# Optimization experiments

Measured on AMD Instinct MI355X. Metric: run time of the kernel, lower is better.

## Reference

```python
import jax, jax.numpy as jnp
import numpy as np

HEADS = 16
DIM_HEAD = 64
CHUNK = 64
EPS_LN = 1e-5
EPS_T5 = 1e-6


def _layernorm(x, g, b):
    mu = x.mean(-1, keepdims=True)
    var = x.var(-1, keepdims=True)
    return (x - mu) / jnp.sqrt(var + EPS_LN) * g + b


def _t5norm(x, w):
    # T5LayerNorm variant: divide by (||x|| * d^-0.5), i.e. RMS norm
    norm = jnp.linalg.norm(x, axis=-1, keepdims=True) * (x.shape[-1] ** -0.5)
    return x / jnp.maximum(norm, EPS_T5) * w


def _rotary(t, freqs):
    rot = freqs.shape[-1]
    t1, t2 = t[..., :rot], t[..., rot:]
    half = rot // 2
    a, b = t1[..., :half], t1[..., half:]
    rh = jnp.concatenate((-b, a), axis=-1)  # rotate_half
    t1 = t1 * jnp.cos(freqs) + rh * jnp.sin(freqs)
    return jnp.concatenate((t1, t2), axis=-1)


def _split_heads(t):
    B, N, _ = t.shape
    return t.reshape(B, N, HEADS, DIM_HEAD).transpose(0, 2, 1, 3)


def _merge_heads(t):
    B, H, N, D = t.shape
    return t.transpose(0, 2, 1, 3).reshape(B, N, H * D)


def _attend(q, k, v, causal=False):
    sim = jnp.einsum('bhid,bhjd->bhij', q, k)
    if causal:
        i, j = sim.shape[-2:]
        m = jnp.triu(jnp.ones((i, j), bool), j - i + 1)
        sim = jnp.where(m, jnp.finfo(sim.dtype).min, sim)
    attn = jax.nn.softmax(sim, axis=-1)
    return jnp.einsum('bhij,bhjd->bhid', attn, v)


def setup_inputs() -> dict:
    key = jax.random.key(0)
    ks = jax.random.split(key, 20)
    b, n, d = 4, 1024, 1024
    kc, r, rn = n // CHUNK, 2, 2 * CHUNK
    dff = 4 * d
    s = 0.02

    def W(i, *shape):
        return jax.random.normal(ks[i], shape, jnp.float32) * s

    return {
        'hidden_states': jax.random.normal(ks[0], (b, n, d), jnp.float32),
        'retrieval': jax.random.normal(ks[1], (b, kc, r, rn, d), jnp.float32),
        'q_pos_emb': jax.random.normal(ks[2], (1, 1, CHUNK, DIM_HEAD), jnp.float32),
        'k_pos_emb': jax.random.normal(ks[3], (1, 1, rn, DIM_HEAD), jnp.float32),
        'ln1_g': jnp.ones(d), 'ln1_b': jnp.zeros(d),
        'Wq_s': W(4, d, d), 'Wk_s': W(5, d, d), 'Wv_s': W(6, d, d),
        'Wo_s': W(7, d, d), 'bo_s': jnp.zeros(d),
        'ln2_g': jnp.ones(d), 'ln2_b': jnp.zeros(d),
        'Wq_c': W(8, d, d), 'Wk_c': W(9, d, d), 'Wv_c': W(10, d, d),
        'Wo_c': W(11, d, d), 'bo_c': jnp.zeros(d),
        'null_k': jax.random.normal(ks[12], (d,), jnp.float32),
        'null_v': jax.random.normal(ks[13], (d,), jnp.float32),
        'post_w': jnp.ones(d),
        'W1': W(14, d, dff), 'b1': jnp.zeros(dff),
        'W2': W(15, dff, d), 'b2': jnp.zeros(d),
    }


def reference(hidden_states, retrieval, q_pos_emb, k_pos_emb,
              ln1_g, ln1_b, Wq_s, Wk_s, Wv_s, Wo_s, bo_s,
              ln2_g, ln2_b, Wq_c, Wk_c, Wv_c, Wo_c, bo_c,
              null_k, null_v, post_w, W1, b1, W2, b2):
    b, n, d = hidden_states.shape
    scale = DIM_HEAD ** -0.5

    # --- causal self-attention (pre-LN) ---
    x = _layernorm(hidden_states, ln1_g, ln1_b)
    q = _split_heads(x @ Wq_s) * scale
    k = _split_heads(x @ Wk_s)
    v = _split_heads(x @ Wv_s)
    o = _merge_heads(_attend(q, k, v, causal=True)) @ Wo_s + bo_s
    hs = _layernorm(o + hidden_states, ln2_g, ln2_b)
    residual = hs  # residual taken after ln_2, before cross-attn (per source)

    # --- chunked cross-attention over retrieved neighbor chunks ---
    kc, r, rn = retrieval.shape[1:4]
    cp = CHUNK - 1  # causal padding
    seq_index = (n // CHUNK) * CHUNK
    # shift queries back by chunk_size-1 (causality), pad tail with zeros
    xq = jnp.pad(hs[:, cp:], ((0, 0), (0, cp), (0, 0)))[:, :seq_index]
    xq = xq.reshape(b * kc, CHUNK, d)
    ctx = retrieval.reshape(b * kc, r * rn, d)
    qpe = jnp.pad(q_pos_emb[:, :, cp:], ((0, 0), (0, 0), (0, cp), (0, 0)))
    kpe = jnp.tile(k_pos_emb, (1, 1, r, 1))  # 'b h n d -> b h (r n) d'
    q = _rotary(_split_heads(xq @ Wq_c) * scale, qpe)
    kk = _rotary(_split_heads(ctx @ Wk_c), kpe)
    vv = _split_heads(ctx @ Wv_c)
    nk = jnp.broadcast_to(null_k.reshape(1, HEADS, 1, DIM_HEAD), (b * kc, HEADS, 1, DIM_HEAD))
    nv = jnp.broadcast_to(null_v.reshape(1, HEADS, 1, DIM_HEAD), (b * kc, HEADS, 1, DIM_HEAD))
    kk = jnp.concatenate((nk, kk), axis=2)
    vv = jnp.concatenate((nv, vv), axis=2)
    cca = _merge_heads(_attend(q, kk, vv)) @ Wo_c + bo_c
    cca = cca.reshape(b, seq_index, d)
    # shift output forward by chunk_size-1, crop to n
    cca = jnp.pad(cca, ((0, 0), (cp, 0), (0, 0)))[:, :n]
    # PostNorm wrapper: T5 norm of (fn(x) + x)
    hs = _t5norm(cca + hs, post_w)

    # --- GPTNeo MLP (gelu-new / tanh approx) ---
    ff = jax.nn.gelu(hs @ W1 + b1, approximate=True) @ W2 + b2
    return residual + ff
```

## Files before the change

kernel.cpp:

```cpp
#include <hip/hip_runtime.h>
#include <hip/hip_bf16.h>
#include <math.h>

using u16 = unsigned short;

static constexpr int SEQ = 1024;
static constexpr int DM  = 1024;
static constexpr int DHD = 64;

typedef __bf16 bfv8 __attribute__((ext_vector_type(8)));
typedef float  f32x4 __attribute__((ext_vector_type(4)));

__device__ __forceinline__ float u2f(u16 u) {
  return __uint_as_float(((unsigned int)u) << 16);
}
__device__ __forceinline__ u16 f2b(float x) {
  __hip_bfloat16 h = __float2bfloat16(x);
  return *reinterpret_cast<u16*>(&h);
}
__device__ __forceinline__ void gload16(const u16* g, u16* l) {
  __builtin_amdgcn_global_load_lds(
      (const __attribute__((address_space(1))) unsigned int*)g,
      (__attribute__((address_space(3))) unsigned int*)l, 16, 0, 0);
}

template <int OT, bool HASBIAS, bool HASRES, bool DOGELU, bool ROT, int DBUF, int PART>
__global__ __launch_bounds__(256) void mgemm_k(
    const u16* __restrict__ A, const u16* __restrict__ Bt, void* __restrict__ C,
    int M, int K, int lda, int ldc, int coff, float alpha0, float alpha1, int acol,
    const float* __restrict__ bias, const float* __restrict__ res,
    const float* __restrict__ tab) {
  constexpr int NBUF = DBUF ? 2 : 1;
  __shared__ u16 As[NBUF][128 * 64];
  __shared__ u16 Bs[NBUF][128 * 64];
  const int tid = threadIdx.x;
  const int w = tid >> 6, lane = tid & 63;
  const int wr = w >> 1, wc = w & 1;
  const int koff = blockIdx.z * K;

  const int nwg = gridDim.x * gridDim.y;
  const int bid = blockIdx.y * gridDim.x + blockIdx.x;
  const int qq = nwg >> 3, r8 = nwg & 7;
  const int xcd = bid & 7, pos = bid >> 3;
  const int cbase = (xcd < r8) ? xcd * (qq + 1) : r8 * (qq + 1) + (xcd - r8) * qq;
  const int logical = cbase + pos;
  const int row0 = (logical / gridDim.x) << 7;
  const int col0 = (logical % gridDim.x) << 7;

  f32x4 acc[4][4] = {};

  auto STAGE = [&](int buf, int k0) {
#pragma unroll
    for (int i = 0; i < 4; ++i) {
      const int c = ((w << 2) + i) * 64 + lane;
      const int r = c >> 3;
      const int cbs = ((c & 7) ^ (r & 7)) << 3;
      const int r64 = r & 63;
      const int rB = (r & 64) | ((r64 & 15) << 2) | (r64 >> 4);
      gload16(A + (size_t)(row0 + r) * lda + koff + k0 + cbs, &As[buf][((w << 2) + i) << 9]);
      gload16(Bt + (size_t)(col0 + rB) * lda + koff + k0 + cbs, &Bs[buf][((w << 2) + i) << 9]);
    }
  };
  auto COMPUTE = [&](int buf) {
#pragma unroll
    for (int kk = 0; kk < 2; ++kk) {
      bfv8 af[4], bfr[4];
#pragma unroll
      for (int m = 0; m < 4; ++m) {
        const int ar = (wr << 6) + (m << 4) + (lane & 15);
        const int sl = ((kk << 2) | (lane >> 4)) ^ (ar & 7);
        af[m] = *reinterpret_cast<const bfv8*>(&As[buf][ar * 64 + (sl << 3)]);
      }
#pragma unroll
      for (int n = 0; n < 4; ++n) {
        const int br = (wc << 6) + (n << 4) + (lane & 15);
        const int sl = ((kk << 2) | (lane >> 4)) ^ (br & 7);
        bfr[n] = *reinterpret_cast<const bfv8*>(&Bs[buf][br * 64 + (sl << 3)]);
      }
#pragma unroll
      for (int m = 0; m < 4; ++m)
#pragma unroll
        for (int n = 0; n < 4; ++n)
          acc[m][n] = __builtin_amdgcn_mfma_f32_16x16x32_bf16(af[m], bfr[n], acc[m][n], 0, 0, 0);
    }
  };

  if constexpr (DBUF) {
    STAGE(0, 0);
    int cur = 0;
    for (int k0 = 0; k0 < K; k0 += 64) {
      if (k0 + 64 < K) {
        STAGE(cur ^ 1, k0 + 64);
        asm volatile("s_waitcnt vmcnt(8)" ::: "memory");
      } else {
        asm volatile("s_waitcnt vmcnt(0)" ::: "memory");
      }
      __builtin_amdgcn_s_barrier();
      __builtin_amdgcn_sched_barrier(0);
      COMPUTE(cur);
      __builtin_amdgcn_s_barrier();
      cur ^= 1;
    }
  } else {
    for (int k0 = 0; k0 < K; k0 += 64) {
      STAGE(0, k0);
      __syncthreads();
      COMPUTE(0);
      __syncthreads();
    }
  }

  const int lr = (lane >> 4) << 2;
  const int lc = lane & 15;
  const int gcb = col0 + (wc << 6) + (lc << 2);
#pragma unroll
  for (int m = 0; m < 4; ++m) {
#pragma unroll
    for (int r = 0; r < 4; ++r) {
      const int gr = row0 + (wr << 6) + (m << 4) + lr + r;
      float t[4];
#pragma unroll
      for (int n = 0; n < 4; ++n)
        t[n] = acc[m][n][r] * ((gcb + n) < acol ? alpha0 : alpha1);
      if constexpr (ROT) {
        const int j = gr & 127;
        const int cc = gcb & 63;
        float4 c4 = *reinterpret_cast<const float4*>(tab + j * 64 + cc);
        float4 s4 = *reinterpret_cast<const float4*>(tab + 8192 + j * 64 + cc);
        const float cs[4] = {c4.x, c4.y, c4.z, c4.w};
        const float sn[4] = {s4.x, s4.y, s4.z, s4.w};
        float o2[4];
#pragma unroll
        for (int n = 0; n < 4; ++n) {
          const float pv = __shfl_xor(t[n], 8);
          const float part = (cc < 32) ? -pv : pv;
          o2[n] = t[n] * cs[n] + part * sn[n];
        }
#pragma unroll
        for (int n = 0; n < 4; ++n) t[n] = o2[n];
      }
      if constexpr (HASBIAS) {
        float4 b4 = *reinterpret_cast<const float4*>(bias + gcb);
        t[0] += b4.x; t[1] += b4.y; t[2] += b4.z; t[3] += b4.w;
      }
      if constexpr (DOGELU) {
#pragma unroll
        for (int n = 0; n < 4; ++n) {
          const float x = t[n];
          t[n] = 0.5f * x * (1.f + tanhf(0.7978845608f * (x + 0.044715f * x * x * x)));
        }
      }
      size_t cb = (size_t)gr * ldc + coff + gcb;
      if constexpr (PART) cb += (size_t)blockIdx.z * M * ldc;
      if constexpr (HASRES) {
        float4 r4 = *reinterpret_cast<const float4*>(res + cb);
        t[0] += r4.x; t[1] += r4.y; t[2] += r4.z; t[3] += r4.w;
      }
      if constexpr (OT == 0) {
        float4 o4 = make_float4(t[0], t[1], t[2], t[3]);
        *reinterpret_cast<float4*>((float*)C + cb) = o4;
      } else {
        ushort4 o4 = {f2b(t[0]), f2b(t[1]), f2b(t[2]), f2b(t[3])};
        *reinterpret_cast<ushort4*>((u16*)C + cb) = o4;
      }
    }
  }
}

__global__ __launch_bounds__(256) void reduce_k(const float* __restrict__ p,
                                                const float* __restrict__ bias,
                                                const float* __restrict__ res,
                                                float* __restrict__ out) {
  const int i = blockIdx.x * 256 + threadIdx.x;
  const int col = (i & 255) << 2;
  float4 a = reinterpret_cast<const float4*>(p)[i];
  float4 b = reinterpret_cast<const float4*>(p + (size_t)4096 * 1024)[i];
  float4 b4 = *reinterpret_cast<const float4*>(bias + col);
  float4 r4 = reinterpret_cast<const float4*>(res)[i];
  float4 o;
  o.x = a.x + b.x + b4.x + r4.x;
  o.y = a.y + b.y + b4.y + r4.y;
  o.z = a.z + b.z + b4.z + r4.z;
  o.w = a.w + b.w + b4.w + r4.w;
  reinterpret_cast<float4*>(out)[i] = o;
}

__global__ __launch_bounds__(256) void costab_k(const float* __restrict__ kpe,
                                                float* __restrict__ tab) {
  const int i = blockIdx.x * 256 + threadIdx.x;
  const float f = kpe[i];
  tab[i] = cosf(f);
  tab[8192 + i] = sinf(f);
}

__global__ __launch_bounds__(256) void wtrans_k(const float* __restrict__ in,
                                                u16* __restrict__ out, int K, int N) {
  __shared__ float t[32][33];
  const int tx = threadIdx.x & 31, ty = threadIdx.x >> 5;
  const int r0 = blockIdx.y << 5, c0 = blockIdx.x << 5;
#pragma unroll
  for (int i = 0; i < 4; ++i)
    t[ty + 8 * i][tx] = in[(size_t)(r0 + ty + 8 * i) * N + c0 + tx];
  __syncthreads();
#pragma unroll
  for (int i = 0; i < 4; ++i)
    out[(size_t)(c0 + ty + 8 * i) * K + r0 + tx] = f2b(t[tx][ty + 8 * i]);
}

__global__ __launch_bounds__(256) void cast_k(const float* __restrict__ in,
                                              u16* __restrict__ out) {
  const int i = blockIdx.x * 256 + threadIdx.x;
  float4 v = reinterpret_cast<const float4*>(in)[i];
  ushort4 o = {f2b(v.x), f2b(v.y), f2b(v.z), f2b(v.w)};
  reinterpret_cast<ushort4*>(out)[i] = o;
}

__global__ __launch_bounds__(256) void ln_k(const float* __restrict__ in,
                                            const float* __restrict__ g,
                                            const float* __restrict__ b,
                                            u16* __restrict__ out) {
  const int tid = threadIdx.x;
  const int c = tid << 2;
  const size_t base = (size_t)blockIdx.x * DM;
  float4 x = *reinterpret_cast<const float4*>(in + base + c);
  float s = x.x + x.y + x.z + x.w;
  float ss = x.x * x.x + x.y * x.y + x.z * x.z + x.w * x.w;
#pragma unroll
  for (int m = 1; m < 64; m <<= 1) {
    s += __shfl_xor(s, m, 64);
    ss += __shfl_xor(ss, m, 64);
  }
  __shared__ float ls[4], lss[4];
  if ((tid & 63) == 0) { ls[tid >> 6] = s; lss[tid >> 6] = ss; }
  __syncthreads();
  s = (ls[0] + ls[1]) + (ls[2] + ls[3]);
  ss = (lss[0] + lss[1]) + (lss[2] + lss[3]);
  const float mu = s * (1.f / DM);
  const float var = ss * (1.f / DM) - mu * mu;
  const float rstd = rsqrtf(var + 1e-5f);
  float4 g4 = *reinterpret_cast<const float4*>(g + c);
  float4 b4 = *reinterpret_cast<const float4*>(b + c);
  ushort4 u;
  u.x = f2b((x.x - mu) * rstd * g4.x + b4.x);
  u.y = f2b((x.y - mu) * rstd * g4.y + b4.y);
  u.z = f2b((x.z - mu) * rstd * g4.z + b4.z);
  u.w = f2b((x.w - mu) * rstd * g4.w + b4.w);
  *reinterpret_cast<ushort4*>(out + base + c) = u;
}

__global__ __launch_bounds__(256) void ln2x_k(const float* __restrict__ in,
                                              const float* __restrict__ g,
                                              const float* __restrict__ b,
                                              float* __restrict__ hs,
                                              u16* __restrict__ xq) {
  const int tid = threadIdx.x;
  const int c = tid << 2;
  const int row = blockIdx.x;
  const size_t base = (size_t)row * DM;
  float4 x = *reinterpret_cast<const float4*>(in + base + c);
  float s = x.x + x.y + x.z + x.w;
  float ss = x.x * x.x + x.y * x.y + x.z * x.z + x.w * x.w;
#pragma unroll
  for (int m = 1; m < 64; m <<= 1) {
    s += __shfl_xor(s, m, 64);
    ss += __shfl_xor(ss, m, 64);
  }
  __shared__ float ls[4], lss[4];
  if ((tid & 63) == 0) { ls[tid >> 6] = s; lss[tid >> 6] = ss; }
  __syncthreads();
  s = (ls[0] + ls[1]) + (ls[2] + ls[3]);
  ss = (lss[0] + lss[1]) + (lss[2] + lss[3]);
  const float mu = s * (1.f / DM);
  const float var = ss * (1.f / DM) - mu * mu;
  const float rstd = rsqrtf(var + 1e-5f);
  float4 g4 = *reinterpret_cast<const float4*>(g + c);
  float4 b4 = *reinterpret_cast<const float4*>(b + c);
  float4 o;
  o.x = (x.x - mu) * rstd * g4.x + b4.x;
  o.y = (x.y - mu) * rstd * g4.y + b4.y;
  o.z = (x.z - mu) * rstd * g4.z + b4.z;
  o.w = (x.w - mu) * rstd * g4.w + b4.w;
  *reinterpret_cast<float4*>(hs + base + c) = o;
  const int local = row & (SEQ - 1);
  const int bb = row >> 10;
  if (local >= 63) {
    ushort4 u = {f2b(o.x), f2b(o.y), f2b(o.z), f2b(o.w)};
    *reinterpret_cast<ushort4*>(xq + (size_t)((bb << 10) + local - 63) * DM + c) = u;
  } else {
    ushort4 z = {0, 0, 0, 0};
    *reinterpret_cast<ushort4*>(xq + (size_t)((bb << 10) + 961 + local) * DM + c) = z;
  }
}

__global__ __launch_bounds__(256) void t5_k(const u16* __restrict__ cca,
                                            const float* __restrict__ hs,
                                            const float* __restrict__ w,
                                            u16* __restrict__ out) {
  const int tid = threadIdx.x;
  const int row = blockIdx.x;
  const int t = row & (SEQ - 1);
  const int c = tid << 2;
  const size_t base = (size_t)row * DM;
  float4 x = *reinterpret_cast<const float4*>(hs + base + c);
  if (t >= 63) {
    ushort4 cu = *reinterpret_cast<const ushort4*>(cca + base - (size_t)63 * DM + c);
    x.x += u2f(cu.x); x.y += u2f(cu.y); x.z += u2f(cu.z); x.w += u2f(cu.w);
  }
  float ss = x.x * x.x + x.y * x.y + x.z * x.z + x.w * x.w;
#pragma unroll
  for (int m = 1; m < 64; m <<= 1) ss += __shfl_xor(ss, m, 64);
  __shared__ float lss[4];
  if ((tid & 63) == 0) lss[tid >> 6] = ss;
  __syncthreads();
  ss = (lss[0] + lss[1]) + (lss[2] + lss[3]);
  const float rms = sqrtf(ss * (1.f / DM));
  const float inv = 1.f / fmaxf(rms, 1e-6f);
  float4 w4 = *reinterpret_cast<const float4*>(w + c);
  ushort4 o = {f2b(x.x * inv * w4.x), f2b(x.y * inv * w4.y),
               f2b(x.z * inv * w4.z), f2b(x.w * inv * w4.w)};
  *reinterpret_cast<ushort4*>(out + base + c) = o;
}

__global__ __launch_bounds__(256) void rotq_k(u16* __restrict__ q,
                                              const float* __restrict__ qpe) {
  __shared__ float rb[DM];
  const size_t base = (size_t)blockIdx.x * 64 * DM;
  const int e = threadIdx.x << 2;
  ushort4 u = *reinterpret_cast<const ushort4*>(q + base + e);
  rb[e + 0] = u2f(u.x); rb[e + 1] = u2f(u.y); rb[e + 2] = u2f(u.z); rb[e + 3] = u2f(u.w);
  __syncthreads();
  u16 ov[4];
#pragma unroll
  for (int k = 0; k < 4; ++k) {
    const int ee = e + k;
    const int cc = ee & 63;
    const float f = qpe[63 * 64 + cc];
    const float t1 = rb[ee];
    const float part = (cc < 32) ? -rb[ee + 32] : rb[ee - 32];
    ov[k] = f2b(t1 * cosf(f) + part * sinf(f));
  }
  ushort4 o = {ov[0], ov[1], ov[2], ov[3]};
  *reinterpret_cast<ushort4*>(q + base + e) = o;
}

__device__ __forceinline__ int vswz(int d, int k) {
  return (k & 7) | (((k >> 3) ^ ((d >> 2) & 7)) << 3);
}

__global__ __launch_bounds__(512) void attn_self_k(const u16* __restrict__ qkv,
                                                   u16* __restrict__ o) {
  const int qt = blockIdx.x, h = blockIdx.y, b = blockIdx.z;
  __shared__ u16 qs[128][72];
  __shared__ u16 ks[64][72];
  __shared__ u16 vt[64][72];
  __shared__ u16 ps[128][72];
  const int tid = threadIdx.x;
  const int w = tid >> 6, lane = tid & 63;
  const int strip = w << 4;
  const int sloc = (w & 3) << 4;
  const int lrow = lane & 15, lk = lane >> 4;
  const int rowb = b * SEQ;
  const int hoff = h * DHD;
  const int qrow0 = qt << 7;

#pragma unroll
  for (int rp = 0; rp < 4; ++rp) {
    const int fi = tid + (rp << 9);
    const int r = fi >> 4, c4 = (fi & 15) << 2;
    *reinterpret_cast<ushort4*>(&qs[r][c4]) =
        *reinterpret_cast<const ushort4*>(qkv + (size_t)(rowb + qrow0 + r) * 3072 + hoff + c4);
  }

  ushort4 kr[2], vr[2];
  auto loadKV = [&](int kt) {
#pragma unroll
    for (int rp = 0; rp < 2; ++rp) {
      const int fi = tid + (rp << 9);
      const int r = fi >> 4, c4 = (fi & 15) << 2;
      const size_t g = (size_t)(rowb + kt * 64 + r) * 3072 + hoff + c4;
      kr[rp] = *reinterpret_cast<const ushort4*>(qkv + g + 1024);
      vr[rp] = *reinterpret_cast<const ushort4*>(qkv + g + 2048);
    }
  };
  loadKV(0);

  const int ktmax = 2 * qt + 1;
  const int ktd = 2 * qt + (w >> 2);

  float mrun[4], lrun[4];
  f32x4 accO[4] = {};
#pragma unroll
  for (int r = 0; r < 4; ++r) { mrun[r] = -1e30f; lrun[r] = 0.f; }

  for (int kt = 0; kt <= ktmax; ++kt) {
    __syncthreads();
#pragma unroll
    for (int rp = 0; rp < 2; ++rp) {
      const int fi = tid + (rp << 9);
      const int r = fi >> 4, c4 = (fi & 15) << 2;
      *reinterpret_cast<ushort4*>(&ks[r][c4]) = kr[rp];
      vt[c4 + 0][vswz(c4 + 0, r)] = vr[rp].x;
      vt[c4 + 1][vswz(c4 + 1, r)] = vr[rp].y;
      vt[c4 + 2][vswz(c4 + 2, r)] = vr[rp].z;
      vt[c4 + 3][vswz(c4 + 3, r)] = vr[rp].w;
    }
    __syncthreads();
    if (kt < ktmax) loadKV(kt + 1);

    if (kt <= ktd) {
      f32x4 sacc[4] = {};
#pragma unroll
      for (int kk = 0; kk < 2; ++kk) {
        bfv8 qf = *reinterpret_cast<const bfv8*>(&qs[strip + lrow][(kk << 5) + (lk << 3)]);
#pragma unroll
        for (int n = 0; n < 4; ++n) {
          bfv8 kf = *reinterpret_cast<const bfv8*>(&ks[(n << 4) + lrow][(kk << 5) + (lk << 3)]);
          sacc[n] = __builtin_amdgcn_mfma_f32_16x16x32_bf16(qf, kf, sacc[n], 0, 0, 0);
        }
      }
      if (kt == ktd) {
#pragma unroll
        for (int n = 0; n < 4; ++n)
#pragma unroll
          for (int r = 0; r < 4; ++r)
            if ((n << 4) + lrow > sloc + (lk << 2) + r) sacc[n][r] = -1e30f;
      }
#pragma unroll
      for (int r = 0; r < 4; ++r) {
        float mt = fmaxf(fmaxf(sacc[0][r], sacc[1][r]), fmaxf(sacc[2][r], sacc[3][r]));
        mt = fmaxf(mt, __shfl_xor(mt, 1));
        mt = fmaxf(mt, __shfl_xor(mt, 2));
        mt = fmaxf(mt, __shfl_xor(mt, 4));
        mt = fmaxf(mt, __shfl_xor(mt, 8));
        const float nm = fmaxf(mrun[r], mt);
        const float f = __expf(mrun[r] - nm);
        mrun[r] = nm;
        float p0 = __expf(sacc[0][r] - nm);
        float p1 = __expf(sacc[1][r] - nm);
        float p2 = __expf(sacc[2][r] - nm);
        float p3 = __expf(sacc[3][r] - nm);
        float rs = (p0 + p1) + (p2 + p3);
        rs += __shfl_xor(rs, 1);
        rs += __shfl_xor(rs, 2);
        rs += __shfl_xor(rs, 4);
        rs += __shfl_xor(rs, 8);
        lrun[r] = lrun[r] * f + rs;
#pragma unroll
        for (int nd = 0; nd < 4; ++nd) accO[nd][r] *= f;
        const int prow = strip + (lk << 2) + r;
        ps[prow][lrow +  0] = f2b(p0);
        ps[prow][lrow + 16] = f2b(p1);
        ps[prow][lrow + 32] = f2b(p2);
        ps[prow][lrow + 48] = f2b(p3);
      }
#pragma unroll
      for (int kk = 0; kk < 2; ++kk) {
        bfv8 pf = *reinterpret_cast<const bfv8*>(&ps[strip + lrow][(kk << 5) + (lk << 3)]);
#pragma unroll
        for (int nd = 0; nd < 4; ++nd) {
          const int vd = (nd << 4) + lrow;
          const int slot = ((kk << 2) | lk) ^ ((vd >> 2) & 7);
          bfv8 vf = *reinterpret_cast<const bfv8*>(&vt[vd][slot << 3]);
          accO[nd] = __builtin_amdgcn_mfma_f32_16x16x32_bf16(pf, vf, accO[nd], 0, 0, 0);
        }
      }
    }
  }
#pragma unroll
  for (int r = 0; r < 4; ++r) {
    const float inv = 1.f / lrun[r];
    const size_t rowoff = (size_t)(rowb + qrow0 + strip + (lk << 2) + r) * DM + hoff;
#pragma unroll
    for (int nd = 0; nd < 4; ++nd)
      o[rowoff + (nd << 4) + lrow] = f2b(accO[nd][r] * inv);
  }
}

__global__ __launch_bounds__(256) void attn_cca_k(
    const u16* __restrict__ q, const u16* __restrict__ kv,
    const float* __restrict__ nullk, const float* __restrict__ nullv,
    u16* __restrict__ o) {
  const int h = blockIdx.y, bk = blockIdx.z;
  __shared__ u16 qs[64][72];
  __shared__ u16 ks[64][72];
  __shared__ u16 vt[64][72];
  __shared__ u16 ps[64][72];
  const int tid = threadIdx.x;
  const int w = tid >> 6, lane = tid & 63;
  const int strip = w << 4;
  const int lrow = lane & 15, lk = lane >> 4;
  const int hoff = h * DHD;
  const size_t qbase = (size_t)bk * 64 * DM + hoff;

#pragma unroll
  for (int rp = 0; rp < 4; ++rp) {
    const int fi = tid + (rp << 8);
    const int r = fi >> 4, c4 = (fi & 15) << 2;
    *reinterpret_cast<ushort4*>(&qs[r][c4]) =
        *reinterpret_cast<const ushort4*>(q + qbase + (size_t)r * DM + c4);
  }

  ushort4 kr[4], vr[4];
  auto loadKV = [&](int kt) {
#pragma unroll
    for (int rp = 0; rp < 4; ++rp) {
      const int fi = tid + (rp << 8);
      const int r = fi >> 4, c4 = (fi & 15) << 2;
      const int kj = kt * 64 + r;
      ushort4 ku = {0, 0, 0, 0}, vu = {0, 0, 0, 0};
      if (kj == 0) {
        float4 nk4 = *reinterpret_cast<const float4*>(nullk + hoff + c4);
        float4 nv4 = *reinterpret_cast<const float4*>(nullv + hoff + c4);
        ku = {f2b(nk4.x), f2b(nk4.y), f2b(nk4.z), f2b(nk4.w)};
        vu = {f2b(nv4.x), f2b(nv4.y), f2b(nv4.z), f2b(nv4.w)};
      } else if (kj <= 256) {
        const size_t g = (size_t)(bk * 256 + kj - 1) * 2048 + hoff + c4;
        ku = *reinterpret_cast<const ushort4*>(kv + g);
        vu = *reinterpret_cast<const ushort4*>(kv + g + 1024);
      }
      kr[rp] = ku; vr[rp] = vu;
    }
  };
  loadKV(0);

  float mrun[4], lrun[4];
  f32x4 accO[4] = {};
#pragma unroll
  for (int r = 0; r < 4; ++r) { mrun[r] = -1e30f; lrun[r] = 0.f; }

  for (int kt = 0; kt < 5; ++kt) {
    __syncthreads();
#pragma unroll
    for (int rp = 0; rp < 4; ++rp) {
      const int fi = tid + (rp << 8);
      const int r = fi >> 4, c4 = (fi & 15) << 2;
      *reinterpret_cast<ushort4*>(&ks[r][c4]) = kr[rp];
      vt[c4 + 0][vswz(c4 + 0, r)] = vr[rp].x;
      vt[c4 + 1][vswz(c4 + 1, r)] = vr[rp].y;
      vt[c4 + 2][vswz(c4 + 2, r)] = vr[rp].z;
      vt[c4 + 3][vswz(c4 + 3, r)] = vr[rp].w;
    }
    __syncthreads();
    if (kt < 4) loadKV(kt + 1);

    f32x4 sacc[4] = {};
#pragma unroll
    for (int kk = 0; kk < 2; ++kk) {
      bfv8 qf = *reinterpret_cast<const bfv8*>(&qs[strip + lrow][(kk << 5) + (lk << 3)]);
#pragma unroll
      for (int n = 0; n < 4; ++n) {
        bfv8 kf = *reinterpret_cast<const bfv8*>(&ks[(n << 4) + lrow][(kk << 5) + (lk << 3)]);
        sacc[n] = __builtin_amdgcn_mfma_f32_16x16x32_bf16(qf, kf, sacc[n], 0, 0, 0);
      }
    }
    if (kt == 4) {
#pragma unroll
      for (int n = 0; n < 4; ++n)
#pragma unroll
        for (int r = 0; r < 4; ++r)
          if ((n << 4) + lrow >= 1) sacc[n][r] = -1e30f;
    }
#pragma unroll
    for (int r = 0; r < 4; ++r) {
      float mt = fmaxf(fmaxf(sacc[0][r], sacc[1][r]), fmaxf(sacc[2][r], sacc[3][r]));
      mt = fmaxf(mt, __shfl_xor(mt, 1));
      mt = fmaxf(mt, __shfl_xor(mt, 2));
      mt = fmaxf(mt, __shfl_xor(mt, 4));
      mt = fmaxf(mt, __shfl_xor(mt, 8));
      const float nm = fmaxf(mrun[r], mt);
      const float f = __expf(mrun[r] - nm);
      mrun[r] = nm;
      float p0 = __expf(sacc[0][r] - nm);
      float p1 = __expf(sacc[1][r] - nm);
      float p2 = __expf(sacc[2][r] - nm);
      float p3 = __expf(sacc[3][r] - nm);
      float rs = (p0 + p1) + (p2 + p3);
      rs += __shfl_xor(rs, 1);
      rs += __shfl_xor(rs, 2);
      rs += __shfl_xor(rs, 4);
      rs += __shfl_xor(rs, 8);
      lrun[r] = lrun[r] * f + rs;
#pragma unroll
      for (int nd = 0; nd < 4; ++nd) accO[nd][r] *= f;
      const int prow = strip + (lk << 2) + r;
      ps[prow][lrow +  0] = f2b(p0);
      ps[prow][lrow + 16] = f2b(p1);
      ps[prow][lrow + 32] = f2b(p2);
      ps[prow][lrow + 48] = f2b(p3);
    }
#pragma unroll
    for (int kk = 0; kk < 2; ++kk) {
      bfv8 pf = *reinterpret_cast<const bfv8*>(&ps[strip + lrow][(kk << 5) + (lk << 3)]);
#pragma unroll
      for (int nd = 0; nd < 4; ++nd) {
        const int vd = (nd << 4) + lrow;
        const int slot = ((kk << 2) | lk) ^ ((vd >> 2) & 7);
        bfv8 vf = *reinterpret_cast<const bfv8*>(&vt[vd][slot << 3]);
        accO[nd] = __builtin_amdgcn_mfma_f32_16x16x32_bf16(pf, vf, accO[nd], 0, 0, 0);
      }
    }
  }
#pragma unroll
  for (int r = 0; r < 4; ++r) {
    const float inv = 1.f / lrun[r];
    const size_t rowoff = (size_t)(bk * 64 + strip + (lk << 2) + r) * DM + hoff;
#pragma unroll
    for (int nd = 0; nd < 4; ++nd)
      o[rowoff + (nd << 4) + lrow] = f2b(accO[nd][r] * inv);
  }
}

extern "C" void kernel_launch(void* const* d_in, const int* in_sizes, int n_in,
                              void* d_out, int out_size, void* d_ws, size_t ws_size,
                              hipStream_t stream) {
  const float* hidden    = (const float*)d_in[0];
  const float* retrieval = (const float*)d_in[1];
  const float* q_pos     = (const float*)d_in[2];
  const float* k_pos     = (const float*)d_in[3];
  const float* ln1_g     = (const float*)d_in[4];
  const float* ln1_b     = (const float*)d_in[5];
  const float* Wq_s      = (const float*)d_in[6];
  const float* Wk_s      = (const float*)d_in[7];
  const float* Wv_s      = (const float*)d_in[8];
  const float* Wo_s      = (const float*)d_in[9];
  const float* bo_s      = (const float*)d_in[10];
  const float* ln2_g     = (const float*)d_in[11];
  const float* ln2_b     = (const float*)d_in[12];
  const float* Wq_c      = (const float*)d_in[13];
  const float* Wk_c      = (const float*)d_in[14];
  const float* Wv_c      = (const float*)d_in[15];
  const float* Wo_c      = (const float*)d_in[16];
  const float* bo_c      = (const float*)d_in[17];
  const float* null_k    = (const float*)d_in[18];
  const float* null_v    = (const float*)d_in[19];
  const float* post_w    = (const float*)d_in[20];
  const float* W1        = (const float*)d_in[21];
  const float* b1        = (const float*)d_in[22];
  const float* W2        = (const float*)d_in[23];
  const float* b2        = (const float*)d_in[24];
  float* out = (float*)d_out;

  constexpr size_t MB = 1024 * 1024;
  constexpr size_t ME = 1024 * 1024;
  char* W = (char*)d_ws;
  u16* Wt_qkv  = (u16*)(W + 0 * MB);
  u16* Wt_os   = (u16*)(W + 6 * MB);
  u16* Wt_qc   = (u16*)(W + 8 * MB);
  u16* Wt_kcvc = (u16*)(W + 10 * MB);
  u16* Wt_oc   = (u16*)(W + 14 * MB);
  u16* W1t     = (u16*)(W + 16 * MB);
  u16* W2t     = (u16*)(W + 24 * MB);
  float* s5    = (float*)(W + 32 * MB);
  float* s0    = (float*)(W + 48 * MB);
  u16* retb    = (u16*)(W + 48 * MB);
  u16* ccab    = (u16*)(W + 48 * MB);
  u16* ccapb   = (u16*)(W + 56 * MB);
  u16* xb      = (u16*)(W + 64 * MB);
  u16* t5b     = (u16*)(W + 64 * MB);
  u16* attnb   = (u16*)(W + 80 * MB);
  u16* xqb     = (u16*)(W + 80 * MB);
  float* tab   = (float*)(W + 80 * MB);
  u16* qkvb    = (u16*)(W + 88 * MB);
  u16* qcb     = (u16*)(W + 88 * MB);
  u16* kkvvb   = (u16*)(W + 96 * MB);
  u16* ff1b    = (u16*)(W + 96 * MB);
  float* fpart = (float*)(W + 128 * MB);

  const dim3 blk(256);

  wtrans_k<<<dim3(32, 32), blk, 0, stream>>>(Wq_s, Wt_qkv + 0 * ME, 1024, 1024);
  wtrans_k<<<dim3(32, 32), blk, 0, stream>>>(Wk_s, Wt_qkv + 1 * ME, 1024, 1024);
  wtrans_k<<<dim3(32, 32), blk, 0, stream>>>(Wv_s, Wt_qkv + 2 * ME, 1024, 1024);
  wtrans_k<<<dim3(32, 32), blk, 0, stream>>>(Wo_s, Wt_os, 1024, 1024);
  wtrans_k<<<dim3(32, 32), blk, 0, stream>>>(Wq_c, Wt_qc, 1024, 1024);
  wtrans_k<<<dim3(32, 32), blk, 0, stream>>>(Wk_c, Wt_kcvc + 0 * ME, 1024, 1024);
  wtrans_k<<<dim3(32, 32), blk, 0, stream>>>(Wv_c, Wt_kcvc + 1 * ME, 1024, 1024);
  wtrans_k<<<dim3(32, 32), blk, 0, stream>>>(Wo_c, Wt_oc, 1024, 1024);
  wtrans_k<<<dim3(128, 32), blk, 0, stream>>>(W1, W1t, 1024, 4096);
  wtrans_k<<<dim3(32, 128), blk, 0, stream>>>(W2, W2t, 4096, 1024);

  ln_k<<<dim3(4096), blk, 0, stream>>>(hidden, ln1_g, ln1_b, xb);
  mgemm_k<1, false, false, false, false, 1, 0><<<dim3(24, 32), blk, 0, stream>>>(
      xb, Wt_qkv, qkvb, 4096, 1024, 1024, 3072, 0, 0.125f, 1.f, 1024, nullptr, nullptr, nullptr);
  attn_self_k<<<dim3(8, 16, 4), dim3(512), 0, stream>>>(qkvb, attnb);
  mgemm_k<0, true, true, false, false, 1, 0><<<dim3(8, 32), blk, 0, stream>>>(
      attnb, Wt_os, s0, 4096, 1024, 1024, 1024, 0, 1.f, 1.f, 0, bo_s, hidden, nullptr);
  ln2x_k<<<dim3(4096), blk, 0, stream>>>(s0, ln2_g, ln2_b, s5, xqb);
  cast_k<<<dim3(16384), blk, 0, stream>>>(retrieval, retb);
  mgemm_k<1, false, false, false, false, 1, 0><<<dim3(8, 32), blk, 0, stream>>>(
      xqb, Wt_qc, qcb, 4096, 1024, 1024, 1024, 0, 1.f, 0.125f, 0, nullptr, nullptr, nullptr);
  rotq_k<<<dim3(64), blk, 0, stream>>>(qcb, q_pos);
  costab_k<<<dim3(32), blk, 0, stream>>>(k_pos, tab);
  mgemm_k<1, false, false, false, true, 0, 0><<<dim3(8, 128), blk, 0, stream>>>(
      retb, Wt_kcvc, kkvvb, 16384, 1024, 1024, 2048, 0, 1.f, 1.f, 0, nullptr, nullptr, tab);
  mgemm_k<1, false, false, false, false, 0, 0><<<dim3(8, 128), blk, 0, stream>>>(
      retb, Wt_kcvc + 1024 * 1024, kkvvb, 16384, 1024, 1024, 2048, 1024, 1.f, 1.f, 0,
      nullptr, nullptr, nullptr);
  attn_cca_k<<<dim3(1, 16, 64), blk, 0, stream>>>(qcb, kkvvb, null_k, null_v, ccab);
  mgemm_k<1, true, false, false, false, 1, 0><<<dim3(8, 32), blk, 0, stream>>>(
      ccab, Wt_oc, ccapb, 4096, 1024, 1024, 1024, 0, 1.f, 1.f, 0, bo_c, nullptr, nullptr);
  t5_k<<<dim3(4096), blk, 0, stream>>>(ccapb, s5, post_w, t5b);
  mgemm_k<1, true, false, true, false, 0, 0><<<dim3(32, 32), blk, 0, stream>>>(
      t5b, W1t, ff1b, 4096, 1024, 1024, 4096, 0, 1.f, 1.f, 0, b1, nullptr, nullptr);
  mgemm_k<0, false, false, false, false, 1, 1><<<dim3(8, 32, 2), blk, 0, stream>>>(
      ff1b, W2t, fpart, 4096, 2048, 4096, 1024, 0, 1.f, 1.f, 0, nullptr, nullptr, nullptr);
  reduce_k<<<dim3(4096), blk, 0, stream>>>(fpart, b2, s5, out);
}
```

Measured before the change: 481.7 us.

## Fuse cross-attention K and V projections into one GEMM sharing A tiles

Result: no change. 491.3 us (+2.0%).

```diff
diff --git a/kernel.cpp b/kernel.cpp
--- a/kernel.cpp
+++ b/kernel.cpp
@@ -163,6 +163,104 @@
         ushort4 o4 = {f2b(t[0]), f2b(t[1]), f2b(t[2]), f2b(t[3])};
         *reinterpret_cast<ushort4*>((u16*)C + cb) = o4;
       }
+    }
+  }
+}
+
+__global__ __launch_bounds__(256) void mgemm_kv_k(
+    const u16* __restrict__ A, const u16* __restrict__ Bt, u16* __restrict__ C,
+    const float* __restrict__ tab) {
+  __shared__ u16 As[128 * 64];
+  __shared__ u16 Bk[128 * 64];
+  __shared__ u16 Bv[128 * 64];
+  const int tid = threadIdx.x;
+  const int w = tid >> 6, lane = tid & 63;
+  const int wr = w >> 1, wc = w & 1;
+
+  const int nwg = gridDim.x * gridDim.y;
+  const int bid = blockIdx.y * gridDim.x + blockIdx.x;
+  const int qq = nwg >> 3, r8 = nwg & 7;
+  const int xcd = bid & 7, pos = bid >> 3;
+  const int cbase = (xcd < r8) ? xcd * (qq + 1) : r8 * (qq + 1) + (xcd - r8) * qq;
+  const int logical = cbase + pos;
+  const int row0 = (logical / gridDim.x) << 7;
+  const int col0 = (logical % gridDim.x) << 7;
+
+  f32x4 ak[4][4] = {};
+  f32x4 av[4][4] = {};
+
+  for (int k0 = 0; k0 < 1024; k0 += 64) {
+#pragma unroll
+    for (int i = 0; i < 4; ++i) {
+      const int c = ((w << 2) + i) * 64 + lane;
+      const int r = c >> 3;
+      const int cbs = ((c & 7) ^ (r & 7)) << 3;
+      const int r64 = r & 63;
+      const int rB = (r & 64) | ((r64 & 15) << 2) | (r64 >> 4);
+      const int lds = ((w << 2) + i) << 9;
+      gload16(A + (size_t)(row0 + r) * 1024 + k0 + cbs, &As[lds]);
+      gload16(Bt + (size_t)(col0 + rB) * 1024 + k0 + cbs, &Bk[lds]);
+      gload16(Bt + (size_t)(1024 + col0 + rB) * 1024 + k0 + cbs, &Bv[lds]);
+    }
+    __syncthreads();
+#pragma unroll
+    for (int kk = 0; kk < 2; ++kk) {
+      bfv8 af[4], bk[4], bv[4];
+#pragma unroll
+      for (int m = 0; m < 4; ++m) {
+        const int ar = (wr << 6) + (m << 4) + (lane & 15);
+        const int sl = ((kk << 2) | (lane >> 4)) ^ (ar & 7);
+        af[m] = *reinterpret_cast<const bfv8*>(&As[ar * 64 + (sl << 3)]);
+      }
+#pragma unroll
+      for (int n = 0; n < 4; ++n) {
+        const int br = (wc << 6) + (n << 4) + (lane & 15);
+        const int sl = ((kk << 2) | (lane >> 4)) ^ (br & 7);
+        bk[n] = *reinterpret_cast<const bfv8*>(&Bk[br * 64 + (sl << 3)]);
+        bv[n] = *reinterpret_cast<const bfv8*>(&Bv[br * 64 + (sl << 3)]);
+      }
+#pragma unroll
+      for (int m = 0; m < 4; ++m)
+#pragma unroll
+        for (int n = 0; n < 4; ++n) {
+          ak[m][n] = __builtin_amdgcn_mfma_f32_16x16x32_bf16(af[m], bk[n], ak[m][n], 0, 0, 0);
+          av[m][n] = __builtin_amdgcn_mfma_f32_16x16x32_bf16(af[m], bv[n], av[m][n], 0, 0, 0);
+        }
+    }
+    __syncthreads();
+  }
+
+  const int lr = (lane >> 4) << 2;
+  const int lc = lane & 15;
+  const int gcb = col0 + (wc << 6) + (lc << 2);
+#pragma unroll
+  for (int m = 0; m < 4; ++m) {
+#pragma unroll
+    for (int r = 0; r < 4; ++r) {
+      const int gr = row0 + (wr << 6) + (m << 4) + lr + r;
+      float t[4];
+#pragma unroll
+      for (int n = 0; n < 4; ++n) t[n] = ak[m][n][r];
+      {
+        const int j = gr & 127;
+        const int cc = gcb & 63;
+        float4 c4 = *reinterpret_cast<const float4*>(tab + j * 64 + cc);
+        float4 s4 = *reinterpret_cast<const float4*>(tab + 8192 + j * 64 + cc);
+        const float cs[4] = {c4.x, c4.y, c4.z, c4.w};
+        const float sn[4] = {s4.x, s4.y, s4.z, s4.w};
+        float o2[4];
+#pragma unroll
+        for (int n = 0; n < 4; ++n) {
+          const float pv = __shfl_xor(t[n], 8);
+          const float part = (cc < 32) ? -pv : pv;
+          o2[n] = t[n] * cs[n] + part * sn[n];
+        }
+        ushort4 o4 = {f2b(o2[0]), f2b(o2[1]), f2b(o2[2]), f2b(o2[3])};
+        *reinterpret_cast<ushort4*>(C + (size_t)gr * 2048 + gcb) = o4;
+      }
+      ushort4 v4 = {f2b(av[m][0][r]), f2b(av[m][1][r]),
+                    f2b(av[m][2][r]), f2b(av[m][3][r])};
+      *reinterpret_cast<ushort4*>(C + (size_t)gr * 2048 + 1024 + gcb) = v4;
     }
   }
 }
@@ -191,6 +289,25 @@
   const float f = kpe[i];
   tab[i] = cosf(f);
   tab[8192 + i] = sinf(f);
+}
+
+struct WtArgs {
+  const float* in[8];
+  u16* out[8];
+};
+__global__ __launch_bounds__(256) void wtrans8_k(WtArgs a) {
+  const float* in = a.in[blockIdx.z];
+  u16* out = a.out[blockIdx.z];
+  __shared__ float t[32][33];
+  const int tx = threadIdx.x & 31, ty = threadIdx.x >> 5;
+  const int r0 = blockIdx.y << 5, c0 = blockIdx.x << 5;
+#pragma unroll
+  for (int i = 0; i < 4; ++i)
+    t[ty + 8 * i][tx] = in[(size_t)(r0 + ty + 8 * i) * 1024 + c0 + tx];
+  __syncthreads();
+#pragma unroll
+  for (int i = 0; i < 4; ++i)
+    out[(size_t)(c0 + ty + 8 * i) * 1024 + r0 + tx] = f2b(t[tx][ty + 8 * i]);
 }
 
 __global__ __launch_bounds__(256) void wtrans_k(const float* __restrict__ in,
@@ -668,14 +785,16 @@
 
   const dim3 blk(256);
 
-  wtrans_k<<<dim3(32, 32), blk, 0, stream>>>(Wq_s, Wt_qkv + 0 * ME, 1024, 1024);
-  wtrans_k<<<dim3(32, 32), blk, 0, stream>>>(Wk_s, Wt_qkv + 1 * ME, 1024, 1024);
-  wtrans_k<<<dim3(32, 32), blk, 0, stream>>>(Wv_s, Wt_qkv + 2 * ME, 1024, 1024);
-  wtrans_k<<<dim3(32, 32), blk, 0, stream>>>(Wo_s, Wt_os, 1024, 1024);
-  wtrans_k<<<dim3(32, 32), blk, 0, stream>>>(Wq_c, Wt_qc, 1024, 1024);
-  wtrans_k<<<dim3(32, 32), blk, 0, stream>>>(Wk_c, Wt_kcvc + 0 * ME, 1024, 1024);
-  wtrans_k<<<dim3(32, 32), blk, 0, stream>>>(Wv_c, Wt_kcvc + 1 * ME, 1024, 1024);
-  wtrans_k<<<dim3(32, 32), blk, 0, stream>>>(Wo_c, Wt_oc, 1024, 1024);
+  WtArgs wa;
+  wa.in[0] = Wq_s; wa.out[0] = Wt_qkv + 0 * ME;
+  wa.in[1] = Wk_s; wa.out[1] = Wt_qkv + 1 * ME;
+  wa.in[2] = Wv_s; wa.out[2] = Wt_qkv + 2 * ME;
+  wa.in[3] = Wo_s; wa.out[3] = Wt_os;
+  wa.in[4] = Wq_c; wa.out[4] = Wt_qc;
+  wa.in[5] = Wk_c; wa.out[5] = Wt_kcvc + 0 * ME;
+  wa.in[6] = Wv_c; wa.out[6] = Wt_kcvc + 1 * ME;
+  wa.in[7] = Wo_c; wa.out[7] = Wt_oc;
+  wtrans8_k<<<dim3(32, 32, 8), blk, 0, stream>>>(wa);
   wtrans_k<<<dim3(128, 32), blk, 0, stream>>>(W1, W1t, 1024, 4096);
   wtrans_k<<<dim3(32, 128), blk, 0, stream>>>(W2, W2t, 4096, 1024);
 
@@ -691,11 +810,7 @@
       xqb, Wt_qc, qcb, 4096, 1024, 1024, 1024, 0, 1.f, 0.125f, 0, nullptr, nullptr, nullptr);
   rotq_k<<<dim3(64), blk, 0, stream>>>(qcb, q_pos);
   costab_k<<<dim3(32), blk, 0, stream>>>(k_pos, tab);
-  mgemm_k<1, false, false, false, true, 0, 0><<<dim3(8, 128), blk, 0, stream>>>(
-      retb, Wt_kcvc, kkvvb, 16384, 1024, 1024, 2048, 0, 1.f, 1.f, 0, nullptr, nullptr, tab);
-  mgemm_k<1, false, false, false, false, 0, 0><<<dim3(8, 128), blk, 0, stream>>>(
-      retb, Wt_kcvc + 1024 * 1024, kkvvb, 16384, 1024, 1024, 2048, 1024, 1.f, 1.f, 0,
-      nullptr, nullptr, nullptr);
+  mgemm_kv_k<<<dim3(8, 128), blk, 0, stream>>>(retb, Wt_kcvc, kkvvb, tab);
   attn_cca_k<<<dim3(1, 16, 64), blk, 0, stream>>>(qcb, kkvvb, null_k, null_v, ccab);
   mgemm_k<1, true, false, false, false, 1, 0><<<dim3(8, 32), blk, 0, stream>>>(
       ccab, Wt_oc, ccapb, 4096, 1024, 1024, 1024, 0, 1.f, 1.f, 0, bo_c, nullptr, nullptr);
```
